# Kernel tuning notes

Hardware: AMD Instinct MI355X
Metric: run time of the kernel (lower is better)

The kernel has to match this reference:

```python
import jax, jax.numpy as jnp
import numpy as np

HEADS = 8
DIM_HEAD = 64
DIM = 256
INNER = HEADS * DIM_HEAD  # 512


def setup_inputs() -> dict:
    key = jax.random.key(0)
    ks = jax.random.split(key, 5)
    b_times_r, n = 32, 1024
    x = jax.random.normal(ks[0], (b_times_r, n, DIM), dtype=jnp.float32)
    # nn.Linear weights stored as (in, out) so y = x @ W
    Wq = jax.random.normal(ks[1], (DIM, INNER), dtype=jnp.float32) * 0.02
    Wkv = jax.random.normal(ks[2], (DIM, 2 * INNER), dtype=jnp.float32) * 0.02
    Wout = jax.random.normal(ks[3], (INNER, DIM), dtype=jnp.float32) * 0.02
    bout = jax.random.normal(ks[4], (DIM,), dtype=jnp.float32) * 0.02
    return {"x": x, "Wq": Wq, "Wkv": Wkv, "Wout": Wout, "bout": bout, "tie_attn_dim": 32}


def reference(x, Wq, Wkv, Wout, bout, tie_attn_dim):
    r = tie_attn_dim
    br, n, _ = x.shape
    b = br // r
    q = x @ Wq                                   # (b*r, n, inner)
    k, v = jnp.split(x @ Wkv, 2, axis=-1)        # (b*r, n, inner) each

    def split_heads(t):
        # (b*r) n (h d) -> b r h n d
        return t.reshape(b, r, n, HEADS, DIM_HEAD).transpose(0, 1, 3, 2, 4)

    q, k, v = map(split_heads, (q, k, v))
    scale = (DIM_HEAD ** -0.5) * (r ** -0.5)
    # tied attention: sum logits over the MSA row dim r
    dots = jnp.einsum('brhid,brhjd->bhij', q, k) * scale  # (b, h, n, n)
    attn = jax.nn.softmax(dots, axis=-1)
    out = jnp.einsum('bhij,brhjd->brhid', attn, v)        # (b, r, h, n, d)
    out = out.transpose(0, 1, 3, 2, 4).reshape(br, n, INNER)
    return out @ Wout + bout
```

## Files before the change

kernel.cpp:

```cpp
#include <hip/hip_runtime.h>
#include <math.h>

typedef unsigned short bf16u;
typedef __attribute__((ext_vector_type(8))) short short8;
typedef __attribute__((ext_vector_type(4))) float f32x4;

__device__ __forceinline__ bf16u f2bf(float f) {
    unsigned int u = __float_as_uint(f);
    u += 0x7fffu + ((u >> 16) & 1u);
    return (bf16u)(u >> 16);
}
__device__ __forceinline__ float bf2f(bf16u h) {
    return __uint_as_float(((unsigned int)h) << 16);
}

__device__ __forceinline__ void gload16(const void* g, void* s) {
    __builtin_amdgcn_global_load_lds((const __attribute__((address_space(1))) void*)g,
                                     (__attribute__((address_space(3))) void*)s, 16, 0, 0);
}

template<int EPI>
__global__ __launch_bounds__(256, 4) void gemm_bt(
    const bf16u* __restrict__ Aall, const bf16u* __restrict__ Ball, int K,
    long strideAz, long strideBz,
    bf16u* __restrict__ D0, bf16u* __restrict__ D1, bf16u* __restrict__ D2,
    float* __restrict__ Df, const float* __restrict__ bias, float scale)
{
    const int gx = gridDim.x, gy = gridDim.y;
    const int nwg = gx * gy * gridDim.z;
    int flat = blockIdx.x + gx * (blockIdx.y + gy * blockIdx.z);
    int swz = (nwg & 7) ? flat : (flat & 7) * (nwg >> 3) + (flat >> 3);
    const int bx = swz % gx;
    const int t1 = swz / gx;
    const int by = t1 % gy;
    const int z  = t1 / gy;

    const int tid = threadIdx.x;
    const int l = tid & 63, w = tid >> 6;
    const int fr = l & 15, fq = l >> 4;
    const int kb = fq * 8;
    const bf16u* A = Aall + (long)z * strideAz;
    const bf16u* B = Ball + (long)z * strideBz;
    const int m0 = by * 128, n0 = bx * 128;

    __shared__ __align__(16) bf16u S[16896];

    f32x4 acc[4][4];
#pragma unroll
    for (int i = 0; i < 4; ++i)
#pragma unroll
        for (int j = 0; j < 4; ++j) acc[i][j] = (f32x4){0.f, 0.f, 0.f, 0.f};

    const long aoff0 = (long)(m0 + w * 16 + fr) * K + kb;
    const long aoff1 = (long)(m0 + (w + 4) * 16 + fr) * K + kb;
    const long boff0 = (long)(n0 + w * 16 + fr) * K + kb;
    const long boff1 = (long)(n0 + (w + 4) * 16 + fr) * K + kb;

    const int wr = w >> 1, wc = w & 1;

#define STAGE(c, k0) do { \
        bf16u* as_ = S + (c) * 4096; \
        bf16u* bs_ = S + 8192 + (c) * 4096; \
        gload16(A + aoff0 + (k0), as_ + w * 512); \
        gload16(A + aoff1 + (k0), as_ + w * 512 + 2048); \
        gload16(B + boff0 + (k0), bs_ + w * 512); \
        gload16(B + boff1 + (k0), bs_ + w * 512 + 2048); \
    } while (0)

    STAGE(0, 0);
    __syncthreads();

    int cur = 0;
    for (int k0 = 0; k0 < K; k0 += 32) {
        if (k0 + 32 < K) STAGE(cur ^ 1, k0 + 32);

        const bf16u* Ac = S + cur * 4096;
        const bf16u* Bc = S + 8192 + cur * 4096;
        short8 af[4], bg[4];
#pragma unroll
        for (int t = 0; t < 4; ++t) {
            af[t] = *(const short8*)(Ac + (wr * 4 + t) * 512 + l * 8);
            bg[t] = *(const short8*)(Bc + (wc * 4 + t) * 512 + l * 8);
        }
#pragma unroll
        for (int mt = 0; mt < 4; ++mt)
#pragma unroll
            for (int nt = 0; nt < 4; ++nt)
                acc[mt][nt] = __builtin_amdgcn_mfma_f32_16x16x32_bf16(
                    af[mt], bg[nt], acc[mt][nt], 0, 0, 0);
        __syncthreads();
        cur ^= 1;
    }
#undef STAGE

    if constexpr (EPI == 1) {
        if (n0 >= 1024) {
#pragma unroll
            for (int mt = 0; mt < 4; ++mt) {
#pragma unroll
                for (int nt = 0; nt < 4; ++nt) {
                    const f32x4 v = acc[mt][nt];
                    const int cl = wc * 64 + nt * 16 + fr;
                    const int rl = wr * 64 + mt * 16 + fq * 4;
                    ushort4 pk;
                    pk.x = f2bf(v[0]); pk.y = f2bf(v[1]);
                    pk.z = f2bf(v[2]); pk.w = f2bf(v[3]);
                    *(ushort4*)(S + cl * 132 + rl) = pk;
                }
            }
            __syncthreads();
            const int c2 = n0 - 1024;
            const int rr = m0 >> 10, i0 = m0 & 1023;
            const int rowt = tid >> 4, c0 = (tid & 15) * 8;
#pragma unroll
            for (int p = 0; p < 8; ++p) {
                const int row = p * 16 + rowt;
                const int col = c2 + row;
                const int h = col >> 6, d = col & 63;
                const ushort4 lo = *(const ushort4*)(S + row * 132 + c0);
                const ushort4 hi = *(const ushort4*)(S + row * 132 + c0 + 4);
                short8 v;
                v[0] = lo.x; v[1] = lo.y; v[2] = lo.z; v[3] = lo.w;
                v[4] = hi.x; v[5] = hi.y; v[6] = hi.z; v[7] = hi.w;
                *(short8*)(D2 + ((long)(h * 2048 + rr * 64 + d) << 10) + i0 + c0) = v;
            }
        } else {
#pragma unroll
            for (int mt = 0; mt < 4; ++mt) {
#pragma unroll
                for (int nt = 0; nt < 4; ++nt) {
                    const int cl = wc * 64 + nt * 16 + fr;
                    const int rl = wr * 64 + mt * 16 + fq * 4;
#pragma unroll
                    for (int r = 0; r < 4; ++r)
                        S[(rl + r) * 132 + cl] = f2bf(acc[mt][nt][r]);
                }
            }
            __syncthreads();
            bf16u* Dqk = (n0 < 512) ? D0 : D1;
            const int hbase = ((n0 < 512) ? n0 : n0 - 512) >> 6;
            const int rr = m0 >> 10, i0 = m0 & 1023;
#pragma unroll
            for (int p = 0; p < 8; ++p) {
                const int idx = p * 256 + tid;
                const int lane8 = idx & 7;
                const int row_o = idx >> 3;
                const int hl = row_o >> 7, il = row_o & 127;
                const int cbase = hl * 64 + lane8 * 8;
                const ushort4 lo = *(const ushort4*)(S + il * 132 + cbase);
                const ushort4 hi = *(const ushort4*)(S + il * 132 + cbase + 4);
                short8 v;
                v[0] = lo.x; v[1] = lo.y; v[2] = lo.z; v[3] = lo.w;
                v[4] = hi.x; v[5] = hi.y; v[6] = hi.z; v[7] = hi.w;
                *(short8*)(Dqk + (((long)((hbase + hl) * 1024 + i0 + il)) << 11)
                           + rr * 64 + lane8 * 8) = v;
            }
        }
    } else {
#pragma unroll
        for (int mt = 0; mt < 4; ++mt) {
#pragma unroll
            for (int nt = 0; nt < 4; ++nt) {
                const f32x4 v = acc[mt][nt];
                const int col = n0 + wc * 64 + nt * 16 + fr;
                const int rbase = m0 + wr * 64 + mt * 16 + fq * 4;
#pragma unroll
                for (int r = 0; r < 4; ++r)
                    Df[(long)(rbase + r) * 256 + col] = v[r] + bias[col];
            }
        }
    }
}

#define MM(a_, b_, c_) c_ = __builtin_amdgcn_mfma_f32_16x16x32_bf16(a_, b_, c_, 0, 0, 0)
#define BAR() __builtin_amdgcn_s_barrier()

#define STG() do { if (q < nht) { \
    const int t_ = q >> 2, p_ = q & 3; \
    const bf16u* P_ = (p_ < 2) ? B : A; \
    const long s_ = ((p_ < 2) ? brow : arow) + ((p_ & 1) ? r128 : 0) + t_ * 64; \
    bf16u* d_ = S + ((t_ & 1) << 15) + ((p_ < 2) ? 16384 : 0) + ((p_ & 1) << 12) + (w << 9); \
    gload16(P_ + s_, d_); \
    gload16(P_ + s_ + 32, d_ + 8192); \
  } ++q; } while (0)

#define RDA(dst, t, m, kk) dst = *(const short8*)(S + (((t) & 1) << 15) + ((kk) << 13) + ((wr * 8 + (m)) << 9) + (l << 3))
#define RDB(dst, t, n, kk) dst = *(const short8*)(S + (((t) & 1) << 15) + 16384 + ((kk) << 13) + ((wc * 4 + (n)) << 9) + (l << 3))

#define KTILE(t, VMASM) do { \
  RDA(af[0][0],t,0,0); RDA(af[0][1],t,0,1); RDA(af[1][0],t,1,0); RDA(af[1][1],t,1,1); \
  RDA(af[2][0],t,2,0); RDA(af[2][1],t,2,1); RDA(af[3][0],t,3,0); RDA(af[3][1],t,3,1); \
  RDB(b0[0][0],t,0,0); RDB(b0[0][1],t,0,1); RDB(b0[1][0],t,1,0); RDB(b0[1][1],t,1,1); \
  STG(); \
  BAR(); \
  __builtin_amdgcn_s_setprio(1); \
  MM(af[0][0],b0[0][0],acc[0][0]); MM(af[0][1],b0[0][1],acc[0][0]); \
  MM(af[0][0],b0[1][0],acc[0][1]); MM(af[0][1],b0[1][1],acc[0][1]); \
  MM(af[1][0],b0[0][0],acc[1][0]); MM(af[1][1],b0[0][1],acc[1][0]); \
  MM(af[1][0],b0[1][0],acc[1][1]); MM(af[1][1],b0[1][1],acc[1][1]); \
  MM(af[2][0],b0[0][0],acc[2][0]); MM(af[2][1],b0[0][1],acc[2][0]); \
  MM(af[2][0],b0[1][0],acc[2][1]); MM(af[2][1],b0[1][1],acc[2][1]); \
  MM(af[3][0],b0[0][0],acc[3][0]); MM(af[3][1],b0[0][1],acc[3][0]); \
  MM(af[3][0],b0[1][0],acc[3][1]); MM(af[3][1],b0[1][1],acc[3][1]); \
  __builtin_amdgcn_s_setprio(0); \
  BAR(); \
  RDB(b1[0][0],t,2,0); RDB(b1[0][1],t,2,1); RDB(b1[1][0],t,3,0); RDB(b1[1][1],t,3,1); \
  STG(); \
  BAR(); \
  __builtin_amdgcn_s_setprio(1); \
  MM(af[0][0],b1[0][0],acc[0][2]); MM(af[0][1],b1[0][1],acc[0][2]); \
  MM(af[0][0],b1[1][0],acc[0][3]); MM(af[0][1],b1[1][1],acc[0][3]); \
  MM(af[1][0],b1[0][0],acc[1][2]); MM(af[1][1],b1[0][1],acc[1][2]); \
  MM(af[1][0],b1[1][0],acc[1][3]); MM(af[1][1],b1[1][1],acc[1][3]); \
  MM(af[2][0],b1[0][0],acc[2][2]); MM(af[2][1],b1[0][1],acc[2][2]); \
  MM(af[2][0],b1[1][0],acc[2][3]); MM(af[2][1],b1[1][1],acc[2][3]); \
  MM(af[3][0],b1[0][0],acc[3][2]); MM(af[3][1],b1[0][1],acc[3][2]); \
  MM(af[3][0],b1[1][0],acc[3][3]); MM(af[3][1],b1[1][1],acc[3][3]); \
  __builtin_amdgcn_s_setprio(0); \
  BAR(); \
  RDA(af[0][0],t,4,0); RDA(af[0][1],t,4,1); RDA(af[1][0],t,5,0); RDA(af[1][1],t,5,1); \
  RDA(af[2][0],t,6,0); RDA(af[2][1],t,6,1); RDA(af[3][0],t,7,0); RDA(af[3][1],t,7,1); \
  STG(); \
  BAR(); \
  __builtin_amdgcn_s_setprio(1); \
  MM(af[0][0],b1[0][0],acc[4][2]); MM(af[0][1],b1[0][1],acc[4][2]); \
  MM(af[0][0],b1[1][0],acc[4][3]); MM(af[0][1],b1[1][1],acc[4][3]); \
  MM(af[1][0],b1[0][0],acc[5][2]); MM(af[1][1],b1[0][1],acc[5][2]); \
  MM(af[1][0],b1[1][0],acc[5][3]); MM(af[1][1],b1[1][1],acc[5][3]); \
  MM(af[2][0],b1[0][0],acc[6][2]); MM(af[2][1],b1[0][1],acc[6][2]); \
  MM(af[2][0],b1[1][0],acc[6][3]); MM(af[2][1],b1[1][1],acc[6][3]); \
  MM(af[3][0],b1[0][0],acc[7][2]); MM(af[3][1],b1[0][1],acc[7][2]); \
  MM(af[3][0],b1[1][0],acc[7][3]); MM(af[3][1],b1[1][1],acc[7][3]); \
  __builtin_amdgcn_s_setprio(0); \
  BAR(); \
  STG(); \
  BAR(); \
  __builtin_amdgcn_s_setprio(1); \
  MM(af[0][0],b0[0][0],acc[4][0]); MM(af[0][1],b0[0][1],acc[4][0]); \
  MM(af[0][0],b0[1][0],acc[4][1]); MM(af[0][1],b0[1][1],acc[4][1]); \
  MM(af[1][0],b0[0][0],acc[5][0]); MM(af[1][1],b0[0][1],acc[5][0]); \
  MM(af[1][0],b0[1][0],acc[5][1]); MM(af[1][1],b0[1][1],acc[5][1]); \
  MM(af[2][0],b0[0][0],acc[6][0]); MM(af[2][1],b0[0][1],acc[6][0]); \
  MM(af[2][0],b0[1][0],acc[6][1]); MM(af[2][1],b0[1][1],acc[6][1]); \
  MM(af[3][0],b0[0][0],acc[7][0]); MM(af[3][1],b0[0][1],acc[7][0]); \
  MM(af[3][0],b0[1][0],acc[7][1]); MM(af[3][1],b0[1][1],acc[7][1]); \
  __builtin_amdgcn_s_setprio(0); \
  VMASM; \
  BAR(); \
} while (0)

template<int EPI>
__global__ __launch_bounds__(512, 2) void gemm8(
    const bf16u* __restrict__ Aall, const bf16u* __restrict__ Ball,
    int Kld, int Kloop, long splitOff, long sAz, long sBz,
    bf16u* __restrict__ D0, float scale)
{
    const int gx = gridDim.x, gy = gridDim.y;
    const int nwg = gx * gy * gridDim.z;
    int flat = blockIdx.x + gx * (blockIdx.y + gy * blockIdx.z);
    int swz = (nwg & 7) ? flat : (flat & 7) * (nwg >> 3) + (flat >> 3);
    const int bx = swz % gx;
    int tq = swz / gx;
    const int by = tq % gy;
    const int z = tq / gy;

    const int tid = threadIdx.x;
    const int l = tid & 63, w = tid >> 6;
    const int fr = l & 15, fq = l >> 4;
    const int wr = w >> 2, wc = w & 3;
    const bf16u* A = Aall + (long)(z & 7) * sAz + (long)(z >> 3) * splitOff;
    const bf16u* B = Ball + (long)(z & 7) * sBz + (long)(z >> 3) * splitOff;
    const int m0 = by << 8, n0 = bx << 8;

    __shared__ __align__(16) bf16u S[65536];

    f32x4 acc[8][4];
#pragma unroll
    for (int i = 0; i < 8; ++i)
#pragma unroll
        for (int j = 0; j < 4; ++j) acc[i][j] = (f32x4){0.f, 0.f, 0.f, 0.f};

    const int NT = Kloop >> 6;
    const int nht = NT << 2;
    const int NI = NT >> 1;
    int q = 0;

    const long arow = (long)(m0 + w * 16 + fr) * Kld + fq * 8;
    const long brow = (long)(n0 + w * 16 + fr) * Kld + fq * 8;
    const long r128 = (long)128 * Kld;

    STG(); STG(); STG(); STG(); STG(); STG();
    asm volatile("s_waitcnt vmcnt(4)" ::: "memory");
    BAR();

    short8 af[4][2], b0[2][2], b1[2][2];

    for (int i = 0; i < NI - 1; ++i) {
        KTILE(2 * i,     asm volatile("s_waitcnt vmcnt(4)" ::: "memory"));
        KTILE(2 * i + 1, asm volatile("s_waitcnt vmcnt(4)" ::: "memory"));
    }
    KTILE(2 * NI - 2, asm volatile("s_waitcnt vmcnt(0)" ::: "memory"));
    KTILE(2 * NI - 1, (void)0);

    const int colb = n0 + wc * 64;
    const int rowb = m0 + wr * 128;
    if constexpr (EPI == 2) {
#pragma unroll
        for (int m = 0; m < 8; ++m)
#pragma unroll
            for (int n = 0; n < 4; ++n) {
                const int col = colb + n * 16 + fr;
                const int rb = rowb + m * 16 + fq * 4;
#pragma unroll
                for (int r = 0; r < 4; ++r)
                    D0[((long)z << 20) + ((long)(rb + r) << 10) + col] = f2bf(acc[m][n][r] * scale);
            }
    } else {
#pragma unroll
        for (int m = 0; m < 8; ++m)
#pragma unroll
            for (int n = 0; n < 4; ++n) {
                const int col = colb + n * 16 + fr;
                const int cb = col >> 6, d = col & 63;
                const int rb = rowb + m * 16 + fq * 4;
#pragma unroll
                for (int r = 0; r < 4; ++r)
                    D0[((long)(cb * 1024 + rb + r) << 9) + (z & 7) * 64 + d] = f2bf(acc[m][n][r]);
            }
    }
}

__global__ __launch_bounds__(256) void cvt_x(const float* __restrict__ in,
                                             bf16u* __restrict__ out) {
    const long idx = (long)(blockIdx.x * 256 + threadIdx.x) * 4;
    const float4 v = *(const float4*)(in + idx);
    ushort4 o;
    o.x = f2bf(v.x); o.y = f2bf(v.y); o.z = f2bf(v.z); o.w = f2bf(v.w);
    *(ushort4*)(out + idx) = o;
}

__global__ __launch_bounds__(256) void transpose_cvt(const float* __restrict__ in,
                                                     bf16u* __restrict__ out,
                                                     int R, int C) {
    const int idx = blockIdx.x * 256 + threadIdx.x;
    if (idx < R * C) {
        const int r = idx / C, c = idx % C;
        out[(long)c * R + r] = f2bf(in[idx]);
    }
}

__global__ __launch_bounds__(256) void softmax_rows2(const bf16u* __restrict__ attP,
                                                     bf16u* __restrict__ att) {
    const long base = (long)blockIdx.x << 10;
    const int tid = threadIdx.x;
    const uint2 u0 = *(const uint2*)(attP + base + tid * 4);
    const uint2 u1 = *(const uint2*)(attP + 8388608 + base + tid * 4);
    const float v0 = bf2f(u0.x & 0xffffu) + bf2f(u1.x & 0xffffu);
    const float v1 = bf2f(u0.x >> 16)     + bf2f(u1.x >> 16);
    const float v2 = bf2f(u0.y & 0xffffu) + bf2f(u1.y & 0xffffu);
    const float v3 = bf2f(u0.y >> 16)     + bf2f(u1.y >> 16);
    float m = fmaxf(fmaxf(v0, v1), fmaxf(v2, v3));
#pragma unroll
    for (int o = 32; o; o >>= 1) m = fmaxf(m, __shfl_xor(m, o));
    __shared__ float red[8];
    if ((tid & 63) == 0) red[tid >> 6] = m;
    __syncthreads();
    m = fmaxf(fmaxf(red[0], red[1]), fmaxf(red[2], red[3]));
    const float e0 = __expf(v0 - m), e1 = __expf(v1 - m);
    const float e2 = __expf(v2 - m), e3 = __expf(v3 - m);
    float s = e0 + e1 + e2 + e3;
#pragma unroll
    for (int o = 32; o; o >>= 1) s += __shfl_xor(s, o);
    if ((tid & 63) == 0) red[4 + (tid >> 6)] = s;
    __syncthreads();
    const float inv = 1.0f / (red[4] + red[5] + red[6] + red[7]);
    uint2 o2;
    o2.x = (unsigned)f2bf(e0 * inv) | ((unsigned)f2bf(e1 * inv) << 16);
    o2.y = (unsigned)f2bf(e2 * inv) | ((unsigned)f2bf(e3 * inv) << 16);
    *(uint2*)(att + base + tid * 4) = o2;
}

extern "C" void kernel_launch(void* const* d_in, const int* in_sizes, int n_in,
                              void* d_out, int out_size, void* d_ws, size_t ws_size,
                              hipStream_t stream) {
    (void)in_sizes; (void)n_in; (void)out_size; (void)ws_size;
    const float* x    = (const float*)d_in[0];
    const float* Wq   = (const float*)d_in[1];
    const float* Wkv  = (const float*)d_in[2];
    const float* Wout = (const float*)d_in[3];
    const float* bout = (const float*)d_in[4];
    float* out = (float*)d_out;

    char* ws = (char*)d_ws;
    bf16u* xb    = (bf16u*)(ws);
    bf16u* WqkvT = (bf16u*)(ws + 16777216);
    bf16u* WoutT = (bf16u*)(ws + 17563648);
    bf16u* Qt    = (bf16u*)(ws + 17825792);
    bf16u* Kt    = (bf16u*)(ws + 51380224);
    bf16u* Vt2   = (bf16u*)(ws + 84934656);
    bf16u* att   = (bf16u*)(ws + 118489088);
    bf16u* out2  = (bf16u*)(ws + 135266304);
    bf16u* attP  = out2;

    cvt_x<<<8192, 256, 0, stream>>>(x, xb);
    transpose_cvt<<<512, 256, 0, stream>>>(Wq, WqkvT, 256, 512);
    transpose_cvt<<<1024, 256, 0, stream>>>(Wkv, WqkvT + 512 * 256, 256, 1024);
    transpose_cvt<<<512, 256, 0, stream>>>(Wout, WoutT, 512, 256);

    const float scale = 1.0f / (8.0f * sqrtf(32.0f));

    gemm_bt<1><<<dim3(12, 256, 1), 256, 0, stream>>>(
        xb, WqkvT, 256, 0, 0, Qt, Kt, Vt2, nullptr, nullptr, 0.f);

    gemm8<2><<<dim3(4, 4, 16), 512, 0, stream>>>(
        Qt, Kt, 2048, 1024, 1024, 1024L * 2048, 1024L * 2048, attP, scale);

    softmax_rows2<<<8192, 256, 0, stream>>>(attP, att);

    gemm8<3><<<dim3(8, 4, 8), 512, 0, stream>>>(
        att, Vt2, 1024, 1024, 0, 1024L * 1024, 2048L * 1024, out2, 0.f);

    gemm_bt<4><<<dim3(2, 256, 1), 256, 0, stream>>>(
        out2, WoutT, 512, 0, 0, nullptr, nullptr, nullptr, out, bout, 0.f);
}
```

Measured before the change: 258.2 us.

## Move QKV projection onto 256x256 gemm8 and stage output GEMM epilogue via LDS

```diff
diff --git a/kernel.cpp b/kernel.cpp
--- a/kernel.cpp
+++ b/kernel.cpp
@@ -17,159 +17,6 @@
 __device__ __forceinline__ void gload16(const void* g, void* s) {
     __builtin_amdgcn_global_load_lds((const __attribute__((address_space(1))) void*)g,
                                      (__attribute__((address_space(3))) void*)s, 16, 0, 0);
-}
-
-template<int EPI>
-__global__ __launch_bounds__(256, 4) void gemm_bt(
-    const bf16u* __restrict__ Aall, const bf16u* __restrict__ Ball, int K,
-    long strideAz, long strideBz,
-    bf16u* __restrict__ D0, bf16u* __restrict__ D1, bf16u* __restrict__ D2,
-    float* __restrict__ Df, const float* __restrict__ bias, float scale)
-{
-    const int gx = gridDim.x, gy = gridDim.y;
-    const int nwg = gx * gy * gridDim.z;
-    int flat = blockIdx.x + gx * (blockIdx.y + gy * blockIdx.z);
-    int swz = (nwg & 7) ? flat : (flat & 7) * (nwg >> 3) + (flat >> 3);
-    const int bx = swz % gx;
-    const int t1 = swz / gx;
-    const int by = t1 % gy;
-    const int z  = t1 / gy;
-
-    const int tid = threadIdx.x;
-    const int l = tid & 63, w = tid >> 6;
-    const int fr = l & 15, fq = l >> 4;
-    const int kb = fq * 8;
-    const bf16u* A = Aall + (long)z * strideAz;
-    const bf16u* B = Ball + (long)z * strideBz;
-    const int m0 = by * 128, n0 = bx * 128;
-
-    __shared__ __align__(16) bf16u S[16896];
-
-    f32x4 acc[4][4];
-#pragma unroll
-    for (int i = 0; i < 4; ++i)
-#pragma unroll
-        for (int j = 0; j < 4; ++j) acc[i][j] = (f32x4){0.f, 0.f, 0.f, 0.f};
-
-    const long aoff0 = (long)(m0 + w * 16 + fr) * K + kb;
-    const long aoff1 = (long)(m0 + (w + 4) * 16 + fr) * K + kb;
-    const long boff0 = (long)(n0 + w * 16 + fr) * K + kb;
-    const long boff1 = (long)(n0 + (w + 4) * 16 + fr) * K + kb;
-
-    const int wr = w >> 1, wc = w & 1;
-
-#define STAGE(c, k0) do { \
-        bf16u* as_ = S + (c) * 4096; \
-        bf16u* bs_ = S + 8192 + (c) * 4096; \
-        gload16(A + aoff0 + (k0), as_ + w * 512); \
-        gload16(A + aoff1 + (k0), as_ + w * 512 + 2048); \
-        gload16(B + boff0 + (k0), bs_ + w * 512); \
-        gload16(B + boff1 + (k0), bs_ + w * 512 + 2048); \
-    } while (0)
-
-    STAGE(0, 0);
-    __syncthreads();
-
-    int cur = 0;
-    for (int k0 = 0; k0 < K; k0 += 32) {
-        if (k0 + 32 < K) STAGE(cur ^ 1, k0 + 32);
-
-        const bf16u* Ac = S + cur * 4096;
-        const bf16u* Bc = S + 8192 + cur * 4096;
-        short8 af[4], bg[4];
-#pragma unroll
-        for (int t = 0; t < 4; ++t) {
-            af[t] = *(const short8*)(Ac + (wr * 4 + t) * 512 + l * 8);
-            bg[t] = *(const short8*)(Bc + (wc * 4 + t) * 512 + l * 8);
-        }
-#pragma unroll
-        for (int mt = 0; mt < 4; ++mt)
-#pragma unroll
-            for (int nt = 0; nt < 4; ++nt)
-                acc[mt][nt] = __builtin_amdgcn_mfma_f32_16x16x32_bf16(
-                    af[mt], bg[nt], acc[mt][nt], 0, 0, 0);
-        __syncthreads();
-        cur ^= 1;
-    }
-#undef STAGE
-
-    if constexpr (EPI == 1) {
-        if (n0 >= 1024) {
-#pragma unroll
-            for (int mt = 0; mt < 4; ++mt) {
-#pragma unroll
-                for (int nt = 0; nt < 4; ++nt) {
-                    const f32x4 v = acc[mt][nt];
-                    const int cl = wc * 64 + nt * 16 + fr;
-                    const int rl = wr * 64 + mt * 16 + fq * 4;
-                    ushort4 pk;
-                    pk.x = f2bf(v[0]); pk.y = f2bf(v[1]);
-                    pk.z = f2bf(v[2]); pk.w = f2bf(v[3]);
-                    *(ushort4*)(S + cl * 132 + rl) = pk;
-                }
-            }
-            __syncthreads();
-            const int c2 = n0 - 1024;
-            const int rr = m0 >> 10, i0 = m0 & 1023;
-            const int rowt = tid >> 4, c0 = (tid & 15) * 8;
-#pragma unroll
-            for (int p = 0; p < 8; ++p) {
-                const int row = p * 16 + rowt;
-                const int col = c2 + row;
-                const int h = col >> 6, d = col & 63;
-                const ushort4 lo = *(const ushort4*)(S + row * 132 + c0);
-                const ushort4 hi = *(const ushort4*)(S + row * 132 + c0 + 4);
-                short8 v;
-                v[0] = lo.x; v[1] = lo.y; v[2] = lo.z; v[3] = lo.w;
-                v[4] = hi.x; v[5] = hi.y; v[6] = hi.z; v[7] = hi.w;
-                *(short8*)(D2 + ((long)(h * 2048 + rr * 64 + d) << 10) + i0 + c0) = v;
-            }
-        } else {
-#pragma unroll
-            for (int mt = 0; mt < 4; ++mt) {
-#pragma unroll
-                for (int nt = 0; nt < 4; ++nt) {
-                    const int cl = wc * 64 + nt * 16 + fr;
-                    const int rl = wr * 64 + mt * 16 + fq * 4;
-#pragma unroll
-                    for (int r = 0; r < 4; ++r)
-                        S[(rl + r) * 132 + cl] = f2bf(acc[mt][nt][r]);
-                }
-            }
-            __syncthreads();
-            bf16u* Dqk = (n0 < 512) ? D0 : D1;
-            const int hbase = ((n0 < 512) ? n0 : n0 - 512) >> 6;
-            const int rr = m0 >> 10, i0 = m0 & 1023;
-#pragma unroll
-            for (int p = 0; p < 8; ++p) {
-                const int idx = p * 256 + tid;
-                const int lane8 = idx & 7;
-                const int row_o = idx >> 3;
-                const int hl = row_o >> 7, il = row_o & 127;
-                const int cbase = hl * 64 + lane8 * 8;
-                const ushort4 lo = *(const ushort4*)(S + il * 132 + cbase);
-                const ushort4 hi = *(const ushort4*)(S + il * 132 + cbase + 4);
-                short8 v;
-                v[0] = lo.x; v[1] = lo.y; v[2] = lo.z; v[3] = lo.w;
-                v[4] = hi.x; v[5] = hi.y; v[6] = hi.z; v[7] = hi.w;
-                *(short8*)(Dqk + (((long)((hbase + hl) * 1024 + i0 + il)) << 11)
-                           + rr * 64 + lane8 * 8) = v;
-            }
-        }
-    } else {
-#pragma unroll
-        for (int mt = 0; mt < 4; ++mt) {
-#pragma unroll
-            for (int nt = 0; nt < 4; ++nt) {
-                const f32x4 v = acc[mt][nt];
-                const int col = n0 + wc * 64 + nt * 16 + fr;
-                const int rbase = m0 + wr * 64 + mt * 16 + fq * 4;
-#pragma unroll
-                for (int r = 0; r < 4; ++r)
-                    Df[(long)(rbase + r) * 256 + col] = v[r] + bias[col];
-            }
-        }
-    }
 }
 
 #define MM(a_, b_, c_) c_ = __builtin_amdgcn_mfma_f32_16x16x32_bf16(a_, b_, c_, 0, 0, 0)
@@ -253,7 +100,8 @@
 __global__ __launch_bounds__(512, 2) void gemm8(
     const bf16u* __restrict__ Aall, const bf16u* __restrict__ Ball,
     int Kld, int Kloop, long splitOff, long sAz, long sBz,
-    bf16u* __restrict__ D0, float scale)
+    bf16u* __restrict__ D0, bf16u* __restrict__ D1, bf16u* __restrict__ D2,
+    float scale)
 {
     const int gx = gridDim.x, gy = gridDim.y;
     const int nwg = gx * gy * gridDim.z;
@@ -304,7 +152,70 @@
 
     const int colb = n0 + wc * 64;
     const int rowb = m0 + wr * 128;
-    if constexpr (EPI == 2) {
+    if constexpr (EPI == 1) {
+        const int rr = m0 >> 10, i0 = m0 & 1023;
+        if (n0 >= 1024) {
+            const int c2 = n0 - 1024;
+#pragma unroll
+            for (int pv = 0; pv < 2; ++pv) {
+                __syncthreads();
+                if ((wc >> 1) == pv) {
+#pragma unroll
+                    for (int m = 0; m < 8; ++m)
+#pragma unroll
+                        for (int n = 0; n < 4; ++n) {
+                            const int cl = (wc & 1) * 64 + n * 16 + fr;
+                            const int rowl = wr * 128 + m * 16 + fq * 4;
+                            ushort4 pk;
+                            pk.x = f2bf(acc[m][n][0]); pk.y = f2bf(acc[m][n][1]);
+                            pk.z = f2bf(acc[m][n][2]); pk.w = f2bf(acc[m][n][3]);
+                            *(ushort4*)(S + cl * 264 + rowl) = pk;
+                        }
+                }
+                __syncthreads();
+#pragma unroll
+                for (int p = 0; p < 8; ++p) {
+                    const int idx = p * 512 + tid;
+                    const int ch = idx >> 5;
+                    const int c8 = (idx & 31) * 8;
+                    const int col = c2 + pv * 128 + ch;
+                    const int h = col >> 6, d = col & 63;
+                    *(short8*)(D2 + ((long)(h * 2048 + rr * 64 + d) << 10) + i0 + c8)
+                        = *(const short8*)(S + ch * 264 + c8);
+                }
+            }
+        } else {
+            bf16u* Dqk = (n0 < 512) ? D0 : D1;
+            const int nq = (n0 < 512) ? n0 : n0 - 512;
+#pragma unroll
+            for (int p2 = 0; p2 < 2; ++p2) {
+                __syncthreads();
+                if (wr == p2) {
+#pragma unroll
+                    for (int m = 0; m < 8; ++m)
+#pragma unroll
+                        for (int n = 0; n < 4; ++n) {
+                            const int cl = wc * 64 + n * 16 + fr;
+                            const int rl = m * 16 + fq * 4;
+#pragma unroll
+                            for (int r = 0; r < 4; ++r)
+                                S[(rl + r) * 264 + cl] = f2bf(acc[m][n][r]);
+                        }
+                }
+                __syncthreads();
+#pragma unroll
+                for (int p = 0; p < 8; ++p) {
+                    const int idx = p * 512 + tid;
+                    const int row = idx >> 5;
+                    const int col = (idx & 31) * 8;
+                    const int h = (nq + col) >> 6, d0 = (nq + col) & 63;
+                    const int il = p2 * 128 + row;
+                    *(short8*)(Dqk + ((long)(h * 1024 + i0 + il) << 11) + rr * 64 + d0)
+                        = *(const short8*)(S + row * 264 + col);
+                }
+            }
+        }
+    } else if constexpr (EPI == 2) {
 #pragma unroll
         for (int m = 0; m < 8; ++m)
 #pragma unroll
@@ -327,6 +238,101 @@
                 for (int r = 0; r < 4; ++r)
                     D0[((long)(cb * 1024 + rb + r) << 9) + (z & 7) * 64 + d] = f2bf(acc[m][n][r]);
             }
+    }
+}
+
+__global__ __launch_bounds__(256, 4) void gemm_out(
+    const bf16u* __restrict__ A, const bf16u* __restrict__ B, int K,
+    float* __restrict__ Df, const float* __restrict__ bias)
+{
+    const int gx = gridDim.x, gy = gridDim.y;
+    const int nwg = gx * gy;
+    int flat = blockIdx.x + gx * blockIdx.y;
+    int swz = (nwg & 7) ? flat : (flat & 7) * (nwg >> 3) + (flat >> 3);
+    const int bx = swz % gx, by = swz / gx;
+
+    const int tid = threadIdx.x;
+    const int l = tid & 63, w = tid >> 6;
+    const int fr = l & 15, fq = l >> 4;
+    const int kb = fq * 8;
+    const int m0 = by * 128, n0 = bx * 128;
+
+    __shared__ __align__(16) bf16u S[16896];
+
+    f32x4 acc[4][4];
+#pragma unroll
+    for (int i = 0; i < 4; ++i)
+#pragma unroll
+        for (int j = 0; j < 4; ++j) acc[i][j] = (f32x4){0.f, 0.f, 0.f, 0.f};
+
+    const long aoff0 = (long)(m0 + w * 16 + fr) * K + kb;
+    const long aoff1 = (long)(m0 + (w + 4) * 16 + fr) * K + kb;
+    const long boff0 = (long)(n0 + w * 16 + fr) * K + kb;
+    const long boff1 = (long)(n0 + (w + 4) * 16 + fr) * K + kb;
+
+    const int wr = w >> 1, wc = w & 1;
+
+#define STAGE(c, k0) do { \
+        bf16u* as_ = S + (c) * 4096; \
+        bf16u* bs_ = S + 8192 + (c) * 4096; \
+        gload16(A + aoff0 + (k0), as_ + w * 512); \
+        gload16(A + aoff1 + (k0), as_ + w * 512 + 2048); \
+        gload16(B + boff0 + (k0), bs_ + w * 512); \
+        gload16(B + boff1 + (k0), bs_ + w * 512 + 2048); \
+    } while (0)
+
+    STAGE(0, 0);
+    __syncthreads();
+
+    int cur = 0;
+    for (int k0 = 0; k0 < K; k0 += 32) {
+        if (k0 + 32 < K) STAGE(cur ^ 1, k0 + 32);
+
+        const bf16u* Ac = S + cur * 4096;
+        const bf16u* Bc = S + 8192 + cur * 4096;
+        short8 af[4], bg[4];
+#pragma unroll
+        for (int t = 0; t < 4; ++t) {
+            af[t] = *(const short8*)(Ac + (wr * 4 + t) * 512 + l * 8);
+            bg[t] = *(const short8*)(Bc + (wc * 4 + t) * 512 + l * 8);
+        }
+#pragma unroll
+        for (int mt = 0; mt < 4; ++mt)
+#pragma unroll
+            for (int nt = 0; nt < 4; ++nt)
+                acc[mt][nt] = __builtin_amdgcn_mfma_f32_16x16x32_bf16(
+                    af[mt], bg[nt], acc[mt][nt], 0, 0, 0);
+        __syncthreads();
+        cur ^= 1;
+    }
+#undef STAGE
+
+    float* Sf = (float*)S;
+#pragma unroll
+    for (int p2 = 0; p2 < 2; ++p2) {
+        __syncthreads();
+        if (wr == p2) {
+#pragma unroll
+            for (int mt = 0; mt < 4; ++mt)
+#pragma unroll
+                for (int nt = 0; nt < 4; ++nt) {
+                    const int cl = wc * 64 + nt * 16 + fr;
+                    const float b = bias[n0 + cl];
+                    const int rl = mt * 16 + fq * 4;
+#pragma unroll
+                    for (int r = 0; r < 4; ++r)
+                        Sf[(rl + r) * 132 + cl] = acc[mt][nt][r] + b;
+                }
+        }
+        __syncthreads();
+#pragma unroll
+        for (int p = 0; p < 8; ++p) {
+            const int idx = p * 256 + tid;
+            const int row = idx >> 5;
+            const int c4 = (idx & 31) * 4;
+            const float4 v = *(const float4*)(Sf + row * 132 + c4);
+            *(float4*)(Df + (long)(m0 + p2 * 64 + row) * 256 + n0 + c4) = v;
+        }
     }
 }
 
@@ -409,17 +415,17 @@
 
     const float scale = 1.0f / (8.0f * sqrtf(32.0f));
 
-    gemm_bt<1><<<dim3(12, 256, 1), 256, 0, stream>>>(
-        xb, WqkvT, 256, 0, 0, Qt, Kt, Vt2, nullptr, nullptr, 0.f);
+    gemm8<1><<<dim3(6, 128, 1), 512, 0, stream>>>(
+        xb, WqkvT, 256, 256, 0, 0, 0, Qt, Kt, Vt2, 0.f);
 
     gemm8<2><<<dim3(4, 4, 16), 512, 0, stream>>>(
-        Qt, Kt, 2048, 1024, 1024, 1024L * 2048, 1024L * 2048, attP, scale);
+        Qt, Kt, 2048, 1024, 1024, 1024L * 2048, 1024L * 2048, attP, nullptr, nullptr, scale);
 
     softmax_rows2<<<8192, 256, 0, stream>>>(attP, att);
 
     gemm8<3><<<dim3(8, 4, 8), 512, 0, stream>>>(
-        att, Vt2, 1024, 1024, 0, 1024L * 1024, 2048L * 1024, out2, 0.f);
-
-    gemm_bt<4><<<dim3(2, 256, 1), 256, 0, stream>>>(
-        out2, WoutT, 512, 0, 0, nullptr, nullptr, nullptr, out, bout, 0.f);
-}
+        att, Vt2, 1024, 1024, 0, 1024L * 1024, 2048L * 1024, out2, nullptr, nullptr, 0.f);
+
+    gemm_out<<<dim3(2, 256, 1), 256, 0, stream>>>(
+        out2, WoutT, 512, out, bout);
+}
```

Result: no change. 255.3 us (-1.2%).
